# Kernel optimization log

Measured on AMD Instinct MI355X. Metric: run time of the kernel, lower is better.

The kernel has to match this reference:

```python
import jax, jax.numpy as jnp
import numpy as np

D_MODEL, D_FF, RANK = 1024, 4096, 128
BATCH, SEQ = 4, 2048


def setup_inputs() -> dict:
    key = jax.random.key(0)
    ks = jax.random.split(key, 9)
    s = 0.02  # typical transformer init scale
    return {
        "x": jax.random.normal(ks[0], (BATCH, SEQ, D_MODEL), jnp.float32),
        "cfc_U": jax.random.normal(ks[1], (D_MODEL, RANK), jnp.float32) * s,
        "cfc_S": jax.random.uniform(ks[2], (RANK,), jnp.float32, 0.5, 1.5),
        "cfc_V": jax.random.normal(ks[3], (D_FF, RANK), jnp.float32) * s,
        "cfc_bias": jax.random.normal(ks[4], (D_FF,), jnp.float32) * s,
        "cproj_U": jax.random.normal(ks[5], (D_FF, RANK), jnp.float32) * s,
        "cproj_S": jax.random.uniform(ks[6], (RANK,), jnp.float32, 0.5, 1.5),
        "cproj_V": jax.random.normal(ks[7], (D_MODEL, RANK), jnp.float32) * s,
        "cproj_bias": jax.random.normal(ks[8], (D_MODEL,), jnp.float32) * s,
    }


def reference(x, cfc_U, cfc_S, cfc_V, cfc_bias, cproj_U, cproj_S, cproj_V, cproj_bias):
    # c_fc_weight = (U * S) @ V^T  -> [d_model, d_ff];  h = x @ c_fc_weight + b
    cfc_w = (cfc_U * cfc_S[None, :]) @ cfc_V.T            # [D_MODEL, D_FF]
    h = jnp.einsum('bsd,df->bsf', x, cfc_w) + cfc_bias    # [B, S, D_FF]
    h = jax.nn.gelu(h, approximate=False)                 # nn.GELU() = exact erf
    cproj_w = (cproj_U * cproj_S[None, :]) @ cproj_V.T    # [D_FF, D_MODEL]
    out = jnp.einsum('bsf,fd->bsd', h, cproj_w) + cproj_bias
    return out
```

## Files before the change

kernel.cpp:

```cpp
#include <hip/hip_runtime.h>
#include <math.h>

#define D_MODEL 1024
#define D_FF    4096
#define RANK    128
#define M_ROWS  8192

typedef _Float16 f16;
typedef _Float16 f16x8 __attribute__((ext_vector_type(8)));
typedef _Float16 f16x4 __attribute__((ext_vector_type(4)));
typedef float    f32x4 __attribute__((ext_vector_type(4)));

#define MFMA16(a, b, c) __builtin_amdgcn_mfma_f32_16x16x32_f16((a), (b), (c), 0, 0, 0)

__device__ __forceinline__ f16x8 ld8(const f16* p) { return *(const f16x8*)p; }

__device__ __forceinline__ f16x8 cvt8(float4 a0, float4 a1) {
    f16x8 r = { (f16)a0.x, (f16)a0.y, (f16)a0.z, (f16)a0.w,
                (f16)a1.x, (f16)a1.y, (f16)a1.z, (f16)a1.w };
    return r;
}

__device__ __forceinline__ float gelu_fast(float v) {
    float u  = v * 0.70710678118654752440f;
    float au = fabsf(u);
    float t  = __builtin_amdgcn_rcpf(__builtin_fmaf(0.3275911f, au, 1.0f));
    float e  = __expf(-au * au);
    float p  = __builtin_fmaf(1.061405429f, t, -1.453152027f);
    p = __builtin_fmaf(p, t, 1.421413741f);
    p = __builtin_fmaf(p, t, -0.284496736f);
    p = __builtin_fmaf(p, t, 0.254829592f);
    float er = __builtin_fmaf(-p * t, e, 1.0f);
    er = copysignf(er, u);
    return 0.5f * v * (1.0f + er);
}

#define GLOAD16(gp, lp) __builtin_amdgcn_global_load_lds(                     \
    (const __attribute__((address_space(1))) void*)(gp),                      \
    (__attribute__((address_space(3))) void*)(lp), 16, 0, 0)

__global__ __launch_bounds__(256) void k_prep(
    const float* __restrict__ cfcU, const float* __restrict__ cfcS,
    const float* __restrict__ cfcV, const float* __restrict__ pjU,
    const float* __restrict__ pjS,  const float* __restrict__ pjV,
    f16* __restrict__ w1T, f16* __restrict__ v1,
    f16* __restrict__ w2T, f16* __restrict__ v2)
{
    __shared__ float tile[32][33];
    const int b = blockIdx.x, t = threadIdx.x;

    if (b < 320) {
        int j = (b * 256 + t) * 8;
        const float* src; f16* dst;
        if (j < 524288) { src = cfcV + j;            dst = v1 + j; }
        else            { src = pjV + (j - 524288);  dst = v2 + (j - 524288); }
        float4 a0 = *(const float4*)src, a1 = *(const float4*)(src + 4);
        *(f16x8*)dst = cvt8(a0, a1);
        return;
    }

    const float* src; const float* S; f16* dst; int R, tb;
    if (b < 448) { src = cfcU; S = cfcS; dst = w1T; R = 1024; tb = b - 320; }
    else         { src = pjU;  S = pjS;  dst = w2T; R = 4096; tb = b - 448; }
    const int td = tb >> 2, tr = tb & 3;

    const int r0 = t >> 3, c0 = (t & 7) * 4;
    float4 v  = *(const float4*)(src + (size_t)(td * 32 + r0) * 128 + tr * 32 + c0);
    float4 sv = *(const float4*)(S + tr * 32 + c0);
    tile[r0][c0 + 0] = v.x * sv.x;
    tile[r0][c0 + 1] = v.y * sv.y;
    tile[r0][c0 + 2] = v.z * sv.z;
    tile[r0][c0 + 3] = v.w * sv.w;
    __syncthreads();

    const int j = t >> 3, i4 = (t & 7) * 4;
    f16x4 o = { (f16)tile[i4 + 0][j], (f16)tile[i4 + 1][j],
                (f16)tile[i4 + 2][j], (f16)tile[i4 + 3][j] };
    *(f16x4*)&dst[(size_t)(tr * 32 + j) * R + td * 32 + i4] = o;
}

__global__ __launch_bounds__(256, 2) void k_t1(
    const float* __restrict__ x, const f16* __restrict__ w1T,
    f16* __restrict__ t1p)
{
    __shared__ __align__(16) char w1s[65536];

    const int tid  = threadIdx.x;
    const int lane = tid & 63;
    const int wv   = tid >> 6;
    const int wm   = wv & 1, wn = wv >> 1;
    const int m0b  = blockIdx.x * 32;
    const int h    = blockIdx.y;
    const int c    = lane & 15, q = lane >> 4;

#define STAGEW(kk)                                                              \
    _Pragma("unroll") for (int i = 0; i < 16; ++i) {                            \
        int r0_  = wv * 32 + i * 2;                                             \
        int row_ = r0_ + (lane >> 5);                                           \
        int col_ = ((lane & 31) * 16) ^ ((row_ & 7) << 4);                      \
        GLOAD16((const char*)w1T + (size_t)row_ * 2048 + h * 1024 +             \
                (kk) * 512 + col_,                                              \
                w1s + r0_ * 512);                                               \
    }

#define LOADX(dst, kc)                                                          \
    _Pragma("unroll") for (int kb = 0; kb < 4; ++kb) {                          \
        const float* px = &x[(size_t)(m0b + wm * 16 + c) * D_MODEL +            \
                             h * 512 + (kc) * 128 + kb * 32 + q * 8];           \
        dst[kb][0] = *(const float4*)px;                                        \
        dst[kb][1] = *(const float4*)(px + 4); }

#define COMPUTEKC(src, sc)                                                      \
    _Pragma("unroll") for (int kb = 0; kb < 4; ++kb) {                          \
        f16x8 af = cvt8(src[kb][0], src[kb][1]);                                \
        _Pragma("unroll") for (int nt = 0; nt < 4; ++nt) {                      \
            int row_ = wn * 64 + nt * 16 + c;                                   \
            f16x8 bf = *(const f16x8*)(w1s + row_ * 512 +                       \
                (((sc) * 256 + kb * 64 + q * 16) ^ ((row_ & 7) << 4)));         \
            acc[nt] = MFMA16(af, bf, acc[nt]); } }

    float4 xa[4][2], xb[4][2];
    LOADX(xa, 0)
    STAGEW(0)
    __syncthreads();

    f32x4 acc[4] = {};
    LOADX(xb, 1)
    COMPUTEKC(xa, 0)
    COMPUTEKC(xb, 1)
    __syncthreads();
    STAGEW(1)
    LOADX(xa, 2)
    __syncthreads();
    LOADX(xb, 3)
    COMPUTEKC(xa, 0)
    COMPUTEKC(xb, 1)

    f16* o = t1p + (size_t)h * (M_ROWS * RANK);
#pragma unroll
    for (int nt = 0; nt < 4; ++nt)
#pragma unroll
        for (int i2 = 0; i2 < 4; ++i2)
            o[(size_t)(m0b + wm * 16 + q * 4 + i2) * RANK + wn * 64 + nt * 16 + c] =
                (f16)acc[nt][i2];
#undef STAGEW
#undef LOADX
#undef COMPUTEKC
}

#define V1OFF 0
#define W2OFF 32768
#define HSOFF 65536
#define HSTR  56

__global__ __launch_bounds__(256, 2) void k_fused(
    const f16* __restrict__ t1p, const f16* __restrict__ v1,
    const float* __restrict__ bfc, const f16* __restrict__ w2T,
    f16* __restrict__ t2p)
{
    __shared__ __align__(16) char smem[72704];

    const int tid  = threadIdx.x;
    const int lane = tid & 63;
    const int wv   = tid >> 6;
    const int wm   = wv & 1, wf = wv >> 1;
    const int c    = lane & 15, q = lane >> 4;

    const int bx  = blockIdx.x;
    const int s   = (bx & 7) >> 2;
    const int mb  = (bx >> 3) * 4 + (bx & 3);
    const int m0b = mb * 32;
    const int fw  = wf * 32;

    f16* hsw = (f16*)(smem + HSOFF + wv * (16 * HSTR * 2));

#define STAGE(bsel, itn) {                                                      \
    const int ft_ = s * 2048 + (itn) * 64;                                      \
    _Pragma("unroll") for (int i = 0; i < 4; ++i) {                             \
        int rb_  = wv * 16 + i * 4;                                             \
        int row_ = rb_ + (lane >> 4);                                           \
        int col_ = ((lane & 15) * 16) ^ ((row_ & 7) << 4);                      \
        GLOAD16((const char*)v1 + (size_t)(ft_ + row_) * 256 + col_,            \
                smem + V1OFF + (bsel) * 16384 + rb_ * 256);                     \
    }                                                                           \
    _Pragma("unroll") for (int i = 0; i < 4; ++i) {                             \
        int rb_  = wv * 32 + i * 8;                                             \
        int row_ = rb_ + (lane >> 3);                                           \
        int col_ = ((lane & 7) * 16) ^ ((row_ & 7) << 4);                       \
        GLOAD16((const char*)w2T + (size_t)row_ * 8192 + (size_t)ft_ * 2 + col_,\
                smem + W2OFF + (bsel) * 16384 + rb_ * 128);                     \
    }                                                                           \
}

    f16x8 a2[4];
#pragma unroll
    for (int kb = 0; kb < 4; ++kb) {
        const size_t off = (size_t)(m0b + wm * 16 + c) * RANK + kb * 32 + q * 8;
        f16x8 p0 = ld8(t1p + off);
        f16x8 p1 = ld8(t1p + (size_t)(M_ROWS * RANK) + off);
#pragma unroll
        for (int e = 0; e < 8; ++e)
            a2[kb][e] = (f16)((float)p0[e] + (float)p1[e]);
    }

    STAGE(0, 0)
    __syncthreads();

    f32x4 c3[8] = {};

#pragma unroll 1
    for (int it = 0; it < 32; ++it) {
        const int cur = it & 1;
        const int ft  = s * 2048 + it * 64;

        float bb[2];
        bb[0] = bfc[ft + fw + c];
        bb[1] = bfc[ft + fw + 16 + c];

        if (it < 31) STAGE(cur ^ 1, it + 1)

        f32x4 c2[2] = {};
#pragma unroll
        for (int nt = 0; nt < 2; ++nt)
#pragma unroll
            for (int kb = 0; kb < 4; ++kb) {
                int row = fw + nt * 16 + c;
                f16x8 bv = *(const f16x8*)(smem + V1OFF + cur * 16384 +
                    row * 256 + ((kb * 64 + q * 16) ^ ((row & 7) << 4)));
                c2[nt] = MFMA16(a2[kb], bv, c2[nt]);
            }

#pragma unroll
        for (int nt = 0; nt < 2; ++nt)
#pragma unroll
            for (int i2 = 0; i2 < 4; ++i2)
                hsw[(q * 4 + i2) * HSTR + nt * 16 + c] =
                    (f16)gelu_fast(c2[nt][i2] + bb[nt]);
        asm volatile("s_waitcnt lgkmcnt(0)" ::: "memory");

        f16x8 a3 = *(const f16x8*)(hsw + c * HSTR + q * 8);
#pragma unroll
        for (int rt = 0; rt < 8; ++rt) {
            int rr = rt * 16 + c;
            f16x8 bw = *(const f16x8*)(smem + W2OFF + cur * 16384 +
                rr * 128 + ((wf * 64 + q * 16) ^ ((c & 7) << 4)));
            c3[rt] = MFMA16(a3, bw, c3[rt]);
        }
        asm volatile("s_waitcnt lgkmcnt(0)" ::: "memory");

        __syncthreads();
    }
#undef STAGE

    float* rbuf = (float*)smem;

    if (wf == 1) {
        float* rb = rbuf + wm * 2112;
#pragma unroll
        for (int rt = 0; rt < 8; ++rt)
#pragma unroll
            for (int i2 = 0; i2 < 4; ++i2)
                rb[(q * 4 + i2) * 132 + rt * 16 + c] = c3[rt][i2];
    }
    __syncthreads();
    if (wf == 0) {
        float* rb = rbuf + wm * 2112;
#pragma unroll
        for (int rt = 0; rt < 8; ++rt)
#pragma unroll
            for (int i2 = 0; i2 < 4; ++i2)
                c3[rt][i2] += rb[(q * 4 + i2) * 132 + rt * 16 + c];
        f16* o = t2p + (size_t)s * (M_ROWS * RANK);
#pragma unroll
        for (int rt = 0; rt < 8; ++rt)
#pragma unroll
            for (int i2 = 0; i2 < 4; ++i2)
                o[(size_t)(m0b + wm * 16 + q * 4 + i2) * RANK + rt * 16 + c] =
                    (f16)c3[rt][i2];
    }
}

__global__ __launch_bounds__(512, 2) void k_out(
    const f16* __restrict__ t2p, const f16* __restrict__ v2,
    const float* __restrict__ bpj, float* __restrict__ out)
{
    __shared__ __align__(16) f16 v2s[256 * 136];

    const int tid  = threadIdx.x;
    const int lane = tid & 63;
    const int wv   = tid >> 6;
    const int wm   = wv & 3, wn = wv >> 2;
    const int m0b  = blockIdx.x * 64;
    const int n0b  = blockIdx.y * 256;
    const int c    = lane & 15, q = lane >> 4;

#pragma unroll
    for (int i8 = 0; i8 < 8; ++i8) {
        int id = i8 * 512 + tid;
        int nn = id >> 4, k8 = id & 15;
        *(f16x8*)&v2s[nn * 136 + k8 * 8] =
            ld8(v2 + (size_t)(n0b + nn) * RANK + k8 * 8);
    }

    f16x8 a[4];
#pragma unroll
    for (int kb = 0; kb < 4; ++kb) {
        const size_t off = (size_t)(m0b + wm * 16 + c) * RANK + kb * 32 + q * 8;
        f16x8 p0 = ld8(t2p + off);
        f16x8 p1 = ld8(t2p + (size_t)(M_ROWS * RANK) + off);
#pragma unroll
        for (int e = 0; e < 8; ++e)
            a[kb][e] = (f16)((float)p0[e] + (float)p1[e]);
    }
    __syncthreads();

    f32x4 acc[8] = {};
#pragma unroll
    for (int nt = 0; nt < 8; ++nt)
#pragma unroll
        for (int kb = 0; kb < 4; ++kb) {
            f16x8 bf = *(const f16x8*)
                &v2s[(wn * 128 + nt * 16 + c) * 136 + kb * 32 + q * 8];
            acc[nt] = MFMA16(a[kb], bf, acc[nt]);
        }

#pragma unroll
    for (int nt = 0; nt < 8; ++nt) {
        float b = bpj[n0b + wn * 128 + nt * 16 + c];
#pragma unroll
        for (int i2 = 0; i2 < 4; ++i2)
            out[(size_t)(m0b + wm * 16 + q * 4 + i2) * D_MODEL +
                n0b + wn * 128 + nt * 16 + c] = acc[nt][i2] + b;
    }
}

extern "C" void kernel_launch(void* const* d_in, const int* in_sizes, int n_in,
                              void* d_out, int out_size, void* d_ws, size_t ws_size,
                              hipStream_t stream) {
    const float* x    = (const float*)d_in[0];
    const float* cfcU = (const float*)d_in[1];
    const float* cfcS = (const float*)d_in[2];
    const float* cfcV = (const float*)d_in[3];
    const float* cfcB = (const float*)d_in[4];
    const float* pjU  = (const float*)d_in[5];
    const float* pjS  = (const float*)d_in[6];
    const float* pjV  = (const float*)d_in[7];
    const float* pjB  = (const float*)d_in[8];
    float* out = (float*)d_out;

    f16* wsf = (f16*)d_ws;
    f16* t1p = wsf;
    f16* t2p = wsf + 2097152;
    f16* w1T = wsf + 4194304;
    f16* v1  = w1T + 131072;
    f16* w2T = v1  + 524288;
    f16* v2  = w2T + 524288;

    k_prep <<<dim3(960), 256, 0, stream>>>(cfcU, cfcS, cfcV, pjU, pjS, pjV,
                                           w1T, v1, w2T, v2);
    k_t1   <<<dim3(M_ROWS / 32, 2), 256, 0, stream>>>(x, w1T, t1p);
    k_fused<<<dim3(512), 256, 0, stream>>>(t1p, v1, cfcB, w2T, t2p);
    k_out  <<<dim3(M_ROWS / 64, D_MODEL / 256), 512, 0, stream>>>(t2p, v2, pjB, out);
}
```

Baseline: 167.1 us.

## Double fused kernel waves, splitting each F-chunk across eight waves

The fused low-rank FFN kernel now runs 512 threads (8 waves) per block instead of 256. Each wave computes one 16-column F slice per iteration instead of two. In the second GEMM each wave feeds a zero-masked A fragment for the half of K it does not own, which wastes MFMA work, and the split-K partial sums are reduced through shared memory in two rounds. The aim is more latency hiding and parallelism, at the cost of redundant MFMAs, extra reduction syncs and higher register pressure from launch bounds of 512×2.

Result: no change. 169.1 us (+1.2%).

```diff
diff --git a/kernel.cpp b/kernel.cpp
--- a/kernel.cpp
+++ b/kernel.cpp
@@ -151,9 +151,9 @@
 #define V1OFF 0
 #define W2OFF 32768
 #define HSOFF 65536
-#define HSTR  56
-
-__global__ __launch_bounds__(256, 2) void k_fused(
+#define HSTR  24
+
+__global__ __launch_bounds__(512, 2) void k_fused(
     const f16* __restrict__ t1p, const f16* __restrict__ v1,
     const float* __restrict__ bfc, const f16* __restrict__ w2T,
     f16* __restrict__ t2p)
@@ -170,21 +170,20 @@
     const int s   = (bx & 7) >> 2;
     const int mb  = (bx >> 3) * 4 + (bx & 3);
     const int m0b = mb * 32;
-    const int fw  = wf * 32;
 
     f16* hsw = (f16*)(smem + HSOFF + wv * (16 * HSTR * 2));
 
 #define STAGE(bsel, itn) {                                                      \
     const int ft_ = s * 2048 + (itn) * 64;                                      \
-    _Pragma("unroll") for (int i = 0; i < 4; ++i) {                             \
-        int rb_  = wv * 16 + i * 4;                                             \
+    _Pragma("unroll") for (int i = 0; i < 2; ++i) {                             \
+        int rb_  = wv * 8 + i * 4;                                              \
         int row_ = rb_ + (lane >> 4);                                           \
         int col_ = ((lane & 15) * 16) ^ ((row_ & 7) << 4);                      \
         GLOAD16((const char*)v1 + (size_t)(ft_ + row_) * 256 + col_,            \
                 smem + V1OFF + (bsel) * 16384 + rb_ * 256);                     \
     }                                                                           \
-    _Pragma("unroll") for (int i = 0; i < 4; ++i) {                             \
-        int rb_  = wv * 32 + i * 8;                                             \
+    _Pragma("unroll") for (int i = 0; i < 2; ++i) {                             \
+        int rb_  = wv * 16 + i * 8;                                             \
         int row_ = rb_ + (lane >> 3);                                           \
         int col_ = ((lane & 7) * 16) ^ ((row_ & 7) << 4);                       \
         GLOAD16((const char*)w2T + (size_t)row_ * 8192 + (size_t)ft_ * 2 + col_,\
@@ -207,43 +206,39 @@
     __syncthreads();
 
     f32x4 c3[8] = {};
+    const f16x8 zf = {};
+    const bool aact = (q >> 1) == (wf & 1);
 
 #pragma unroll 1
     for (int it = 0; it < 32; ++it) {
         const int cur = it & 1;
         const int ft  = s * 2048 + it * 64;
 
-        float bb[2];
-        bb[0] = bfc[ft + fw + c];
-        bb[1] = bfc[ft + fw + 16 + c];
+        float bb = bfc[ft + wf * 16 + c];
 
         if (it < 31) STAGE(cur ^ 1, it + 1)
 
-        f32x4 c2[2] = {};
-#pragma unroll
-        for (int nt = 0; nt < 2; ++nt)
-#pragma unroll
-            for (int kb = 0; kb < 4; ++kb) {
-                int row = fw + nt * 16 + c;
-                f16x8 bv = *(const f16x8*)(smem + V1OFF + cur * 16384 +
-                    row * 256 + ((kb * 64 + q * 16) ^ ((row & 7) << 4)));
-                c2[nt] = MFMA16(a2[kb], bv, c2[nt]);
-            }
-
-#pragma unroll
-        for (int nt = 0; nt < 2; ++nt)
-#pragma unroll
-            for (int i2 = 0; i2 < 4; ++i2)
-                hsw[(q * 4 + i2) * HSTR + nt * 16 + c] =
-                    (f16)gelu_fast(c2[nt][i2] + bb[nt]);
+        f32x4 c2 = {};
+#pragma unroll
+        for (int kb = 0; kb < 4; ++kb) {
+            int row = wf * 16 + c;
+            f16x8 bv = *(const f16x8*)(smem + V1OFF + cur * 16384 +
+                row * 256 + ((kb * 64 + q * 16) ^ ((row & 7) << 4)));
+            c2 = MFMA16(a2[kb], bv, c2);
+        }
+
+#pragma unroll
+        for (int i2 = 0; i2 < 4; ++i2)
+            hsw[(q * 4 + i2) * HSTR + c] = (f16)gelu_fast(c2[i2] + bb);
         asm volatile("s_waitcnt lgkmcnt(0)" ::: "memory");
 
-        f16x8 a3 = *(const f16x8*)(hsw + c * HSTR + q * 8);
+        f16x8 h8 = *(const f16x8*)(hsw + c * HSTR + (q & 1) * 8);
+        f16x8 a3 = aact ? h8 : zf;
 #pragma unroll
         for (int rt = 0; rt < 8; ++rt) {
             int rr = rt * 16 + c;
             f16x8 bw = *(const f16x8*)(smem + W2OFF + cur * 16384 +
-                rr * 128 + ((wf * 64 + q * 16) ^ ((c & 7) << 4)));
+                rr * 128 + (((wf >> 1) * 64 + q * 16) ^ ((rr & 7) << 4)));
             c3[rt] = MFMA16(a3, bw, c3[rt]);
         }
         asm volatile("s_waitcnt lgkmcnt(0)" ::: "memory");
@@ -254,22 +249,26 @@
 
     float* rbuf = (float*)smem;
 
-    if (wf == 1) {
-        float* rb = rbuf + wm * 2112;
-#pragma unroll
-        for (int rt = 0; rt < 8; ++rt)
-#pragma unroll
-            for (int i2 = 0; i2 < 4; ++i2)
-                rb[(q * 4 + i2) * 132 + rt * 16 + c] = c3[rt][i2];
-    }
+#define ST_C3(rg)                                                               \
+    { float* rb = rbuf + (rg) * 2112;                                           \
+      _Pragma("unroll") for (int rt = 0; rt < 8; ++rt)                          \
+      _Pragma("unroll") for (int i2 = 0; i2 < 4; ++i2)                          \
+          rb[(q * 4 + i2) * 132 + rt * 16 + c] = c3[rt][i2]; }
+#define ADD_C3(rg)                                                              \
+    { float* rb = rbuf + (rg) * 2112;                                           \
+      _Pragma("unroll") for (int rt = 0; rt < 8; ++rt)                          \
+      _Pragma("unroll") for (int i2 = 0; i2 < 4; ++i2)                          \
+          c3[rt][i2] += rb[(q * 4 + i2) * 132 + rt * 16 + c]; }
+
+    __syncthreads();
+    if (wf >= 2) ST_C3(wm * 2 + (wf - 2))
+    __syncthreads();
+    if (wf < 2) ADD_C3(wm * 2 + wf)
+    __syncthreads();
+    if (wf == 1) ST_C3(wm * 2)
     __syncthreads();
     if (wf == 0) {
-        float* rb = rbuf + wm * 2112;
-#pragma unroll
-        for (int rt = 0; rt < 8; ++rt)
-#pragma unroll
-            for (int i2 = 0; i2 < 4; ++i2)
-                c3[rt][i2] += rb[(q * 4 + i2) * 132 + rt * 16 + c];
+        ADD_C3(wm * 2)
         f16* o = t2p + (size_t)s * (M_ROWS * RANK);
 #pragma unroll
         for (int rt = 0; rt < 8; ++rt)
@@ -278,6 +277,8 @@
                 o[(size_t)(m0b + wm * 16 + q * 4 + i2) * RANK + rt * 16 + c] =
                     (f16)c3[rt][i2];
     }
+#undef ST_C3
+#undef ADD_C3
 }
 
 __global__ __launch_bounds__(512, 2) void k_out(
@@ -359,6 +360,6 @@
     k_prep <<<dim3(960), 256, 0, stream>>>(cfcU, cfcS, cfcV, pjU, pjS, pjV,
                                            w1T, v1, w2T, v2);
     k_t1   <<<dim3(M_ROWS / 32, 2), 256, 0, stream>>>(x, w1T, t1p);
-    k_fused<<<dim3(512), 256, 0, stream>>>(t1p, v1, cfcB, w2T, t2p);
+    k_fused<<<dim3(512), 512, 0, stream>>>(t1p, v1, cfcB, w2T, t2p);
     k_out  <<<dim3(M_ROWS / 64, D_MODEL / 256), 512, 0, stream>>>(t2p, v2, pjB, out);
 }
```
